# Performance work log

Measured on AMD Instinct MI355X. Metric: run time of the kernel, lower is better.

The kernel has to match this reference:

```python
import jax, jax.numpy as jnp
import numpy as np

LOG_CLAMP = -100.0  # torch BCELoss clamps each log term at -100


def setup_inputs() -> dict:
    key = jax.random.key(0)
    k1, k2, k3 = jax.random.split(key, 3)
    B, N, W, H = 256, 32, 1920, 1080
    pred_x = jax.random.uniform(k1, (B, N, W), dtype=jnp.float32)
    pred_y = jax.random.uniform(k2, (B, N, H), dtype=jnp.float32)
    target_ball_position = jax.random.randint(k3, (B, N, 2), 0, 1080, dtype=jnp.int64)
    return {"pred_x": pred_x, "pred_y": pred_y,
            "target_ball_position": target_ball_position}


def _axis_bce(pred, tgt):
    """Per-(b,n) mean BCE against an implicit one-hot target along last axis.

    pred: [B, N, L] probabilities; tgt: [B, N] int indices (already clamped).
    Returns [B, N] losses. Avoids materializing the one-hot:
      mean_i BCE_i = (-log p[t] - sum_{i != t} log(1 - p[i])) / L
    with torch-style clamping of each log term at -100.
    """
    L = pred.shape[-1]
    lp = jnp.maximum(jnp.log(pred), LOG_CLAMP)          # [B,N,L]
    l1p = jnp.maximum(jnp.log1p(-pred), LOG_CLAMP)      # [B,N,L]
    t = tgt[..., None]                                   # [B,N,1]
    lp_t = jnp.take_along_axis(lp, t, axis=-1)[..., 0]   # [B,N]
    l1p_t = jnp.take_along_axis(l1p, t, axis=-1)[..., 0]
    sum_l1p = jnp.sum(l1p, axis=-1)                      # [B,N]
    return (-lp_t - (sum_l1p - l1p_t)) / L


def reference(pred_x, pred_y, target_ball_position):
    W = pred_x.shape[2]
    H = pred_y.shape[2]
    tx = jnp.clip(target_ball_position[..., 0].astype(jnp.int32), 0, W - 1)  # [B,N]
    ty = jnp.clip(target_ball_position[..., 1].astype(jnp.int32), 0, H - 1)
    valid = jnp.logical_not((tx == 0) & (ty == 0))       # [B,N]
    vmask = valid.astype(pred_x.dtype)
    loss_x = _axis_bce(pred_x, tx)                       # [B,N]
    loss_y = _axis_bce(pred_y, ty)
    valid_count = jnp.sum(vmask)
    total_x = jnp.sum(loss_x * vmask)
    total_y = jnp.sum(loss_y * vmask)
    denom = jnp.maximum(valid_count, 1.0)  # if count==0 totals are 0 anyway
    return total_x / denom + total_y / denom
```

## Files before the change

### kernel.cpp

```cpp
#include <hip/hip_runtime.h>

#define WDIM 1920
#define HDIM 1080
#define TPB 256
#define PPB 4

__device__ __forceinline__ float clog1m(float p) {
    return fmaxf(__log2f(1.f - p) * 0.69314718056f, -100.f);
}
__device__ __forceinline__ float clog(float p) {
    return fmaxf(__log2f(p) * 0.69314718056f, -100.f);
}

__global__ __launch_bounds__(TPB) void bce_main(const float* __restrict__ px,
                                                const float* __restrict__ py,
                                                const int* __restrict__ tgt,
                                                float* __restrict__ partial_loss,
                                                float* __restrict__ partial_cnt) {
    const int t = threadIdx.x;
    float acc = 0.f;
    float cnt = 0.f;
    const int p0 = blockIdx.x * PPB;

    for (int k = 0; k < PPB; ++k) {
        const int pair = p0 + k;
        int tx = tgt[pair * 2 + 0];
        int ty = tgt[pair * 2 + 1];
        tx = min(max(tx, 0), WDIM - 1);
        ty = min(max(ty, 0), HDIM - 1);
        const float vm = (tx == 0 && ty == 0) ? 0.f : 1.f;

        const float4* rx = (const float4*)(px + (size_t)pair * WDIM);
        const float4* ry = (const float4*)(py + (size_t)pair * HDIM);
        const float4 z4 = make_float4(0.f, 0.f, 0.f, 0.f);

        float4 a0 = rx[t];
        float4 a1 = (t < WDIM / 4 - TPB) ? rx[t + TPB] : z4;
        float4 b0 = ry[t];
        float4 b1 = (t < HDIM / 4 - TPB) ? ry[t + TPB] : z4;

        float sx = clog1m(a0.x) + clog1m(a0.y) + clog1m(a0.z) + clog1m(a0.w)
                 + clog1m(a1.x) + clog1m(a1.y) + clog1m(a1.z) + clog1m(a1.w);
        float sy = clog1m(b0.x) + clog1m(b0.y) + clog1m(b0.z) + clog1m(b0.w)
                 + clog1m(b1.x) + clog1m(b1.y) + clog1m(b1.z) + clog1m(b1.w);

        float corr = 0.f;
        if (t == 0) {
            float pt = px[(size_t)pair * WDIM + tx];
            float qt = py[(size_t)pair * HDIM + ty];
            corr = (clog1m(pt) - clog(pt)) * (1.f / WDIM)
                 + (clog1m(qt) - clog(qt)) * (1.f / HDIM);
            cnt += vm;
        }
        acc += vm * (corr - sx * (1.f / WDIM) - sy * (1.f / HDIM));
    }

    #pragma unroll
    for (int o = 32; o > 0; o >>= 1) acc += __shfl_down(acc, o, 64);
    __shared__ float red[TPB / 64];
    if ((t & 63) == 0) red[t >> 6] = acc;
    __syncthreads();
    if (t == 0) {
        float bs = red[0] + red[1] + red[2] + red[3];
        partial_loss[blockIdx.x] = bs;
        partial_cnt[blockIdx.x]  = cnt;
    }
}

__global__ __launch_bounds__(TPB) void bce_final(const float* __restrict__ pl,
                                                 const float* __restrict__ pc,
                                                 int nblk, float* __restrict__ out) {
    const int t = threadIdx.x;
    float s = 0.f, c = 0.f;
    for (int i = t; i < nblk; i += TPB) { s += pl[i]; c += pc[i]; }
    #pragma unroll
    for (int o = 32; o > 0; o >>= 1) {
        s += __shfl_down(s, o, 64);
        c += __shfl_down(c, o, 64);
    }
    __shared__ float rs[TPB / 64], rc[TPB / 64];
    if ((t & 63) == 0) { rs[t >> 6] = s; rc[t >> 6] = c; }
    __syncthreads();
    if (t == 0) {
        float ts = rs[0] + rs[1] + rs[2] + rs[3];
        float tc = rc[0] + rc[1] + rc[2] + rc[3];
        out[0] = ts / fmaxf(tc, 1.f);
    }
}

extern "C" void kernel_launch(void* const* d_in, const int* in_sizes, int n_in,
                              void* d_out, int out_size, void* d_ws, size_t ws_size,
                              hipStream_t stream) {
    const float* px = (const float*)d_in[0];
    const float* py = (const float*)d_in[1];
    const int* tgt  = (const int*)d_in[2];
    float* out = (float*)d_out;

    const int pairs = in_sizes[0] / WDIM;
    const int nblk  = pairs / PPB;

    float* pl = (float*)d_ws;
    float* pc = pl + nblk;

    bce_main<<<dim3(nblk), dim3(TPB), 0, stream>>>(px, py, tgt, pl, pc);
    bce_final<<<1, TPB, 0, stream>>>(pl, pc, nblk, out);
}
```

Measured before the change: 116.0 us.

## Flatten BCE reduction into grid-stride loop over float4 elements

Result: no change. 118.0 us (+1.8%).

```diff
diff --git a/kernel.cpp b/kernel.cpp
--- a/kernel.cpp
+++ b/kernel.cpp
@@ -3,7 +3,10 @@
 #define WDIM 1920
 #define HDIM 1080
 #define TPB 256
-#define PPB 4
+#define NBLK 2048
+#define PAIRS 8192
+#define X4 (PAIRS * (WDIM / 4))
+#define Y4 (PAIRS * (HDIM / 4))
 
 __device__ __forceinline__ float clog1m(float p) {
     return fmaxf(__log2f(1.f - p) * 0.69314718056f, -100.f);
@@ -14,56 +17,61 @@
 
 __global__ __launch_bounds__(TPB) void bce_main(const float* __restrict__ px,
                                                 const float* __restrict__ py,
-                                                const int* __restrict__ tgt,
+                                                const int2* __restrict__ tgt,
                                                 float* __restrict__ partial_loss,
                                                 float* __restrict__ partial_cnt) {
+    const int tid = blockIdx.x * TPB + threadIdx.x;
+    const int stride = NBLK * TPB;
     const int t = threadIdx.x;
     float acc = 0.f;
     float cnt = 0.f;
-    const int p0 = blockIdx.x * PPB;
 
-    for (int k = 0; k < PPB; ++k) {
-        const int pair = p0 + k;
-        int tx = tgt[pair * 2 + 0];
-        int ty = tgt[pair * 2 + 1];
-        tx = min(max(tx, 0), WDIM - 1);
-        ty = min(max(ty, 0), HDIM - 1);
-        const float vm = (tx == 0 && ty == 0) ? 0.f : 1.f;
+    if (tid < PAIRS) {
+        int2 t2 = tgt[tid];
+        int tx = min(max(t2.x, 0), WDIM - 1);
+        int ty = min(max(t2.y, 0), HDIM - 1);
+        if (!(tx == 0 && ty == 0)) {
+            float pt = px[(size_t)tid * WDIM + tx];
+            float qt = py[(size_t)tid * HDIM + ty];
+            acc += (clog1m(pt) - clog(pt)) * (1.f / WDIM)
+                 + (clog1m(qt) - clog(qt)) * (1.f / HDIM);
+            cnt = 1.f;
+        }
+    }
 
-        const float4* rx = (const float4*)(px + (size_t)pair * WDIM);
-        const float4* ry = (const float4*)(py + (size_t)pair * HDIM);
-        const float4 z4 = make_float4(0.f, 0.f, 0.f, 0.f);
+    const float4* px4 = (const float4*)px;
+    const float4* py4 = (const float4*)py;
 
-        float4 a0 = rx[t];
-        float4 a1 = (t < WDIM / 4 - TPB) ? rx[t + TPB] : z4;
-        float4 b0 = ry[t];
-        float4 b1 = (t < HDIM / 4 - TPB) ? ry[t + TPB] : z4;
-
-        float sx = clog1m(a0.x) + clog1m(a0.y) + clog1m(a0.z) + clog1m(a0.w)
-                 + clog1m(a1.x) + clog1m(a1.y) + clog1m(a1.z) + clog1m(a1.w);
-        float sy = clog1m(b0.x) + clog1m(b0.y) + clog1m(b0.z) + clog1m(b0.w)
-                 + clog1m(b1.x) + clog1m(b1.y) + clog1m(b1.z) + clog1m(b1.w);
-
-        float corr = 0.f;
-        if (t == 0) {
-            float pt = px[(size_t)pair * WDIM + tx];
-            float qt = py[(size_t)pair * HDIM + ty];
-            corr = (clog1m(pt) - clog(pt)) * (1.f / WDIM)
-                 + (clog1m(qt) - clog(qt)) * (1.f / HDIM);
-            cnt += vm;
-        }
-        acc += vm * (corr - sx * (1.f / WDIM) - sy * (1.f / HDIM));
+    for (int i = tid; i < X4; i += stride) {
+        float4 v = px4[i];
+        int pair = i / 480;
+        int2 t2 = tgt[pair];
+        int tx = min(max(t2.x, 0), WDIM - 1);
+        int ty = min(max(t2.y, 0), HDIM - 1);
+        float w = (tx == 0 && ty == 0) ? 0.f : -(1.f / WDIM);
+        acc += w * (clog1m(v.x) + clog1m(v.y) + clog1m(v.z) + clog1m(v.w));
+    }
+    for (int i = tid; i < Y4; i += stride) {
+        float4 v = py4[i];
+        int pair = i / 270;
+        int2 t2 = tgt[pair];
+        int tx = min(max(t2.x, 0), WDIM - 1);
+        int ty = min(max(t2.y, 0), HDIM - 1);
+        float w = (tx == 0 && ty == 0) ? 0.f : -(1.f / HDIM);
+        acc += w * (clog1m(v.x) + clog1m(v.y) + clog1m(v.z) + clog1m(v.w));
     }
 
     #pragma unroll
-    for (int o = 32; o > 0; o >>= 1) acc += __shfl_down(acc, o, 64);
-    __shared__ float red[TPB / 64];
-    if ((t & 63) == 0) red[t >> 6] = acc;
+    for (int o = 32; o > 0; o >>= 1) {
+        acc += __shfl_down(acc, o, 64);
+        cnt += __shfl_down(cnt, o, 64);
+    }
+    __shared__ float rs[TPB / 64], rc[TPB / 64];
+    if ((t & 63) == 0) { rs[t >> 6] = acc; rc[t >> 6] = cnt; }
     __syncthreads();
     if (t == 0) {
-        float bs = red[0] + red[1] + red[2] + red[3];
-        partial_loss[blockIdx.x] = bs;
-        partial_cnt[blockIdx.x]  = cnt;
+        partial_loss[blockIdx.x] = rs[0] + rs[1] + rs[2] + rs[3];
+        partial_cnt[blockIdx.x]  = rc[0] + rc[1] + rc[2] + rc[3];
     }
 }
 
@@ -93,15 +101,12 @@
                               hipStream_t stream) {
     const float* px = (const float*)d_in[0];
     const float* py = (const float*)d_in[1];
-    const int* tgt  = (const int*)d_in[2];
+    const int2* tgt = (const int2*)d_in[2];
     float* out = (float*)d_out;
 
-    const int pairs = in_sizes[0] / WDIM;
-    const int nblk  = pairs / PPB;
+    float* pl = (float*)d_ws;
+    float* pc = pl + NBLK;
 
-    float* pl = (float*)d_ws;
-    float* pc = pl + nblk;
-
-    bce_main<<<dim3(nblk), dim3(TPB), 0, stream>>>(px, py, tgt, pl, pc);
-    bce_final<<<1, TPB, 0, stream>>>(pl, pc, nblk, out);
+    bce_main<<<dim3(NBLK), dim3(TPB), 0, stream>>>(px, py, tgt, pl, pc);
+    bce_final<<<1, TPB, 0, stream>>>(pl, pc, NBLK, out);
 }
```
